# Optimization experiments

Hardware: AMD Instinct MI355X
Metric: run time of the kernel (lower is better)

The kernel has to match this reference:

```python
import jax, jax.numpy as jnp
import numpy as np

N = 50000
E = 800000
IN, HID, OUT = 256, 128, 64
BN_EPS = 1e-5

def sage(x, src, dst, Wl, bl, Wr):
    # PyG SAGEConv (aggr='mean'): lin_l(mean_j x_j) + lin_r(x_root)
    agg = jax.ops.segment_sum(x[src], dst, num_segments=N)
    deg = jax.ops.segment_sum(jnp.ones((src.shape[0], 1), x.dtype), dst, num_segments=N)
    mean_agg = agg / jnp.maximum(deg, 1.0)
    return mean_agg @ Wl + bl + x @ Wr

def bn_eval(x, gamma, beta):
    # eval-mode BatchNorm1d with running_mean=0, running_var=1
    return x * (gamma / jnp.sqrt(1.0 + BN_EPS)) + beta

def setup_inputs() -> dict:
    key = jax.random.key(0)
    ks = jax.random.split(key, 16)
    g = lambda k, shp, s: jax.random.normal(k, shp, jnp.float32) * s
    inp = {
        'x': g(ks[0], (N, IN), 1.0),
        'edge_index': jax.random.randint(ks[1], (2, E), 0, N, jnp.int32),
        'eps': g(ks[2], (10, N, OUT), 1.0),
        'W1l': g(ks[3], (IN, HID), 0.06), 'b1': jnp.zeros((HID,), jnp.float32), 'W1r': g(ks[4], (IN, HID), 0.06),
        'g1': jnp.ones((HID,), jnp.float32), 'be1': jnp.zeros((HID,), jnp.float32),
        'W2l': g(ks[5], (HID, 2 * HID), 0.09), 'b2': jnp.zeros((2 * HID,), jnp.float32), 'W2r': g(ks[6], (HID, 2 * HID), 0.09),
        'g2': jnp.ones((2 * HID,), jnp.float32), 'be2': jnp.zeros((2 * HID,), jnp.float32),
        'W3l': g(ks[7], (2 * HID, 2 * OUT), 0.06), 'b3': jnp.zeros((2 * OUT,), jnp.float32), 'W3r': g(ks[8], (2 * HID, 2 * OUT), 0.06),
        'Wd1': g(ks[9], (OUT, HID), 0.12), 'bd1': jnp.zeros((HID,), jnp.float32),
        'g3': jnp.ones((HID,), jnp.float32), 'be3': jnp.zeros((HID,), jnp.float32),
        'Wd2': g(ks[10], (HID, IN), 0.09), 'bd2': jnp.zeros((IN,), jnp.float32),
    }
    return inp

def reference(x, edge_index, eps, W1l, b1, W1r, g1, be1, W2l, b2, W2r, g2, be2,
              W3l, b3, W3r, Wd1, bd1, g3, be3, Wd2, bd2):
    src, dst = edge_index[0], edge_index[1]
    # encode (dropout is identity in eval mode)
    x1 = bn_eval(jax.nn.relu(sage(x, src, dst, W1l, b1, W1r)), g1, be1)
    x2 = bn_eval(jax.nn.relu(sage(x1, src, dst, W2l, b2, W2r)), g2, be2)
    mz = sage(x2, src, dst, W3l, b3, W3r)
    mean, log_std = mz[:, :OUT], mz[:, OUT:]
    # reparameterize: average of n_samples draws == mean + std * mean(eps)
    std = jnp.exp(log_std)
    z = mean + std * jnp.mean(eps, axis=0)
    # decode
    h = bn_eval(jax.nn.relu(z @ Wd1 + bd1), g3, be3) + x1
    return h @ Wd2 + bd2
```

## Files before the change

kernel.cpp:

```cpp
#include <hip/hip_runtime.h>


typedef unsigned short u16;
typedef short bf16x8 __attribute__((ext_vector_type(8)));
typedef float f32x4  __attribute__((ext_vector_type(4)));

constexpr float BN_EPS = 1e-5f;

__device__ __forceinline__ u16 f2bf(float f) {
    unsigned u = __float_as_uint(f);
    return (u16)((u + 0x7FFFu + ((u >> 16) & 1u)) >> 16);
}
__device__ __forceinline__ float bf2f(u16 h) {
    return __uint_as_float(((unsigned)h) << 16);
}
__device__ __forceinline__ void gl_lds16(const void* g, void* l) {
    __builtin_amdgcn_global_load_lds(
        (const __attribute__((address_space(1))) unsigned*)g,
        (__attribute__((address_space(3))) unsigned*)l, 16, 0, 0);
}

template<int KS>
__device__ __forceinline__ void stage_panel(const u16* g, char* lb, int k0, int t) {
    const int sr   = t >> 2;
    const int sq   = (t & 3) ^ ((t >> 3) & 3);
    const int wave = t >> 6;
    gl_lds16(g + (size_t)sr * KS + k0 + sq * 8,        lb + wave * 1024);
    gl_lds16(g + (size_t)(sr + 64) * KS + k0 + sq * 8, lb + 4096 + wave * 1024);
}


__global__ void histpack(const int* __restrict__ dst, int E, int* __restrict__ deg,
                         const float* __restrict__ x,
                         const float* __restrict__ W1l, const float* __restrict__ W1r,
                         const float* __restrict__ W2l, const float* __restrict__ W2r,
                         const float* __restrict__ W3l, const float* __restrict__ W3r,
                         const float* __restrict__ Wd1, const float* __restrict__ Wd2,
                         u16* __restrict__ Bt1, u16* __restrict__ Bt2,
                         u16* __restrict__ Bt3, u16* __restrict__ Btd1,
                         u16* __restrict__ Btd2, u16* __restrict__ xb,
                         int N, int Mpad) {
    int idx = blockIdx.x * 256 + threadIdx.x;
    if (idx < E) atomicAdd(&deg[dst[idx]], 1);
    if (idx < 65536) {
        int c = idx >> 8, k = idx & 255;
        float v = (c < 128) ? W1l[k * 128 + c] : W1r[k * 128 + (c - 128)];
        Bt1[c * 256 + k] = f2bf(v);
    } else if (idx < 131072) {
        int i2 = idx - 65536;
        int c = i2 >> 8, k = i2 & 255;
        float v = (k < 128) ? W2l[k * 256 + c] : W2r[(k - 128) * 256 + c];
        Bt2[c * 256 + k] = f2bf(v);
    } else if (idx < 196608) {
        int i2 = idx - 131072;
        int c = i2 >> 8, k = i2 & 255;
        float v = (c < 128) ? W3l[k * 128 + c] : W3r[k * 128 + (c - 128)];
        Bt3[c * 256 + k] = f2bf(v);
    } else if (idx < 204800) {
        int i2 = idx - 196608;
        int c = i2 >> 6, k = i2 & 63;
        Btd1[i2] = f2bf(Wd1[k * 128 + c]);
    } else if (idx < 237568) {
        int i2 = idx - 204800;
        int c = i2 >> 7, k = i2 & 127;
        Btd2[i2] = f2bf(Wd2[k * 256 + c]);
    }
    if (idx < Mpad * 64) {
        int row = idx >> 6, q = idx & 63;
        float4 v = make_float4(0.f, 0.f, 0.f, 0.f);
        if (row < N) v = *(const float4*)&x[(size_t)row * 256 + q * 4];
        ushort4 o;
        o.x = f2bf(v.x); o.y = f2bf(v.y); o.z = f2bf(v.z); o.w = f2bf(v.w);
        *(ushort4*)&xb[(size_t)row * 256 + q * 4] = o;
    }
}

__global__ __launch_bounds__(256)
void scan_partial(const int* __restrict__ deg, int N, int* __restrict__ bsum) {
    __shared__ int sd[256];
    int i = blockIdx.x * 256 + threadIdx.x;
    int v = (i < N) ? deg[i] : 0;
    sd[threadIdx.x] = v;
    __syncthreads();
    for (int off = 128; off > 0; off >>= 1) {
        if (threadIdx.x < off) sd[threadIdx.x] += sd[threadIdx.x + off];
        __syncthreads();
    }
    if (threadIdx.x == 0) bsum[blockIdx.x] = sd[0];
}

__global__ __launch_bounds__(256)
void scan_final2(const int* __restrict__ deg, const int* __restrict__ bsum,
                 int N, int E, int* __restrict__ row_ptr, int* __restrict__ cursor,
                 float* __restrict__ inv_deg) {
    __shared__ int sd[256];
    int t = threadIdx.x;
    int partial = 0;
    for (int j = t; j < blockIdx.x; j += 256) partial += bsum[j];
    sd[t] = partial;
    __syncthreads();
    for (int off = 128; off > 0; off >>= 1) {
        if (t < off) sd[t] += sd[t + off];
        __syncthreads();
    }
    int base = sd[0];
    __syncthreads();
    int i = blockIdx.x * 256 + t;
    int d = (i < N) ? deg[i] : 0;
    sd[t] = d;
    __syncthreads();
    for (int off = 1; off < 256; off <<= 1) {
        int u = (t >= off) ? sd[t - off] : 0;
        __syncthreads();
        sd[t] += u;
        __syncthreads();
    }
    if (i < N) {
        int excl = base + sd[t] - d;
        row_ptr[i] = excl;
        cursor[i]  = excl;
        inv_deg[i] = 1.0f / (float)max(d, 1);
        if (i == N - 1) row_ptr[N] = E;
    }
}

__global__ void fill_kernel(const int* __restrict__ src, const int* __restrict__ dst,
                            int E, int* __restrict__ cursor, int* __restrict__ csr) {
    int e = blockIdx.x * 256 + threadIdx.x;
    if (e < E) {
        int p = atomicAdd(&cursor[dst[e]], 1);
        csr[p] = src[e];
    }
}


template<int K, int NC>
__global__ __launch_bounds__(256)
void mgemm(const u16* __restrict__ A, const u16* __restrict__ Bt,
           void* __restrict__ Cout, int M) {
    __shared__ char lds[32768];
    char* As0 = lds;
    char* As1 = lds + 8192;
    char* Bs0 = lds + 16384;
    char* Bs1 = lds + 24576;

    const int t = threadIdx.x;
    const int l = t & 63;
    const int wave = t >> 6;
    const int wr = wave >> 1, wc = wave & 1;
    const int lr = l & 15, kg = l >> 4;
    const int row0 = blockIdx.x * 128;
    const int col0 = blockIdx.y * 128;

    f32x4 acc[4][4];
    #pragma unroll
    for (int m = 0; m < 4; m++)
        #pragma unroll
        for (int n = 0; n < 4; n++)
            #pragma unroll
            for (int r = 0; r < 4; r++) acc[m][n][r] = 0.f;

    const u16* Ab = A  + (size_t)row0 * K;
    const u16* Bb = Bt + (size_t)col0 * K;

    stage_panel<K>(Ab, As0, 0, t);
    stage_panel<K>(Bb, Bs0, 0, t);
    __syncthreads();

    const int swz = (kg ^ ((lr >> 1) & 3)) << 4;
    constexpr int NT = K / 32;
    for (int ks = 0; ks < NT; ks++) {
        char* Ac = (ks & 1) ? As1 : As0;
        char* Bc = (ks & 1) ? Bs1 : Bs0;
        if (ks + 1 < NT) {
            stage_panel<K>(Ab, (ks & 1) ? As0 : As1, (ks + 1) * 32, t);
            stage_panel<K>(Bb, (ks & 1) ? Bs0 : Bs1, (ks + 1) * 32, t);
        }
        bf16x8 af[4], bfr[4];
        #pragma unroll
        for (int m = 0; m < 4; m++)
            af[m] = *(const bf16x8*)(Ac + wr * 4096 + m * 1024 + lr * 64 + swz);
        #pragma unroll
        for (int n = 0; n < 4; n++)
            bfr[n] = *(const bf16x8*)(Bc + wc * 4096 + n * 1024 + lr * 64 + swz);
        #pragma unroll
        for (int m = 0; m < 4; m++)
            #pragma unroll
            for (int n = 0; n < 4; n++)
                acc[m][n] = __builtin_amdgcn_mfma_f32_16x16x32_bf16(
                    af[m], bfr[n], acc[m][n], 0, 0, 0);
        __syncthreads();
    }

    const int colb = col0 + wc * 64;
    const int rowb = row0 + wr * 64;
    __syncthreads();

    char* rp = lds + wave * 4096;
    #pragma unroll
    for (int m = 0; m < 4; m++) {
        #pragma unroll
        for (int n = 0; n < 4; n++)
            #pragma unroll
            for (int r = 0; r < 4; r++) {
                int rl = kg * 4 + r, cl = n * 16 + lr;
                ((u16*)rp)[rl * 64 + cl] = f2bf(acc[m][n][r]);
            }
        u16* rph = (u16*)rp;
        #pragma unroll
        for (int hh = 0; hh < 2; hh++) {
            int rloc = hh * 8 + (l >> 3);
            int grow = rowb + m * 16 + rloc;
            bf16x8 v8 = *(bf16x8*)&rph[rloc * 64 + (l & 7) * 8];
            if (grow < M)
                *(bf16x8*)((u16*)Cout + (size_t)grow * NC + colb + (l & 7) * 8) = v8;
        }
    }
}


__global__ __launch_bounds__(256)
void gemm23(const u16* __restrict__ catX, const u16* __restrict__ Bt2,
            const u16* __restrict__ Bt3,
            const float* __restrict__ b2, const float* __restrict__ g2,
            const float* __restrict__ be2,
            u16* __restrict__ Y3, int M) {
    __shared__ char lds[73728];
    char* Ad0 = lds;
    char* Ad1 = lds + 4096;
    char* Bd0 = lds + 8192;
    char* Bd1 = lds + 8192 + 16384;
    char* hb  = lds + 40960;

    const int t = threadIdx.x;
    const int l = t & 63;
    const int wave = t >> 6;
    const int lr = l & 15, kg = l >> 4;
    const int row0 = blockIdx.x * 64;
    const int swz = (kg ^ ((lr >> 1) & 3)) << 4;
    const int sr = t >> 2;
    const int sq = (t & 3) ^ ((t >> 3) & 3);
    const float rs = rsqrtf(1.0f + BN_EPS);

    const u16* Ab = catX + (size_t)row0 * 256;

    auto stageA = [&](char* buf, int k0) {
        gl_lds16(Ab + (size_t)sr * 256 + k0 + sq * 8, buf + wave * 1024);
    };
    auto stageB = [&](const u16* Bt, char* buf, int k0) {
        #pragma unroll
        for (int q = 0; q < 4; q++)
            gl_lds16(Bt + (size_t)(q * 64 + sr) * 256 + k0 + sq * 8,
                     buf + q * 4096 + wave * 1024);
    };

    f32x4 acc[4][4];
    #pragma unroll
    for (int m = 0; m < 4; m++)
        #pragma unroll
        for (int n = 0; n < 4; n++)
            #pragma unroll
            for (int r = 0; r < 4; r++) acc[m][n][r] = 0.f;

    stageA(Ad0, 0);
    stageB(Bt2, Bd0, 0);
    __syncthreads();
    for (int ks = 0; ks < 8; ks++) {
        char* Ac = (ks & 1) ? Ad1 : Ad0;
        char* Bc = (ks & 1) ? Bd1 : Bd0;
        if (ks < 7) {
            stageA((ks & 1) ? Ad0 : Ad1, (ks + 1) * 32);
            stageB(Bt2, (ks & 1) ? Bd0 : Bd1, (ks + 1) * 32);
        }
        bf16x8 af[4], bfr[4];
        #pragma unroll
        for (int m = 0; m < 4; m++)
            af[m] = *(const bf16x8*)(Ac + m * 1024 + lr * 64 + swz);
        #pragma unroll
        for (int n = 0; n < 4; n++)
            bfr[n] = *(const bf16x8*)(Bc + wave * 4096 + n * 1024 + lr * 64 + swz);
        #pragma unroll
        for (int m = 0; m < 4; m++)
            #pragma unroll
            for (int n = 0; n < 4; n++)
                acc[m][n] = __builtin_amdgcn_mfma_f32_16x16x32_bf16(
                    af[m], bfr[n], acc[m][n], 0, 0, 0);
        __syncthreads();
    }

    stageB(Bt3, Bd0, 0);

    {
        float bia[4], gpr[4], bet[4];
        #pragma unroll
        for (int n = 0; n < 4; n++) {
            int c = wave * 64 + n * 16 + lr;
            bia[n] = b2[c];
            gpr[n] = g2[c] * rs;
            bet[n] = be2[c];
        }
        #pragma unroll
        for (int m = 0; m < 4; m++)
            #pragma unroll
            for (int n = 0; n < 4; n++)
                #pragma unroll
                for (int r = 0; r < 4; r++) {
                    int rl = m * 16 + kg * 4 + r;
                    int cl = wave * 64 + n * 16 + lr;
                    float v = acc[m][n][r] + bia[n];
                    v = fmaxf(v, 0.f) * gpr[n] + bet[n];
                    int slot = (cl >> 3) ^ (rl & 7);
                    ((u16*)(hb + rl * 512 + slot * 16))[cl & 7] = f2bf(v);
                }
    }
    __syncthreads();

    #pragma unroll
    for (int m = 0; m < 4; m++)
        #pragma unroll
        for (int n = 0; n < 4; n++)
            #pragma unroll
            for (int r = 0; r < 4; r++) acc[m][n][r] = 0.f;

    for (int ks = 0; ks < 8; ks++) {
        char* Bc = (ks & 1) ? Bd1 : Bd0;
        if (ks < 7) stageB(Bt3, (ks & 1) ? Bd0 : Bd1, (ks + 1) * 32);
        bf16x8 af[4], bfr[4];
        #pragma unroll
        for (int m = 0; m < 4; m++) {
            int row = m * 16 + lr;
            int s = (ks * 4 + kg) ^ (row & 7);
            af[m] = *(const bf16x8*)(hb + row * 512 + s * 16);
        }
        #pragma unroll
        for (int n = 0; n < 4; n++)
            bfr[n] = *(const bf16x8*)(Bc + wave * 4096 + n * 1024 + lr * 64 + swz);
        #pragma unroll
        for (int m = 0; m < 4; m++)
            #pragma unroll
            for (int n = 0; n < 4; n++)
                acc[m][n] = __builtin_amdgcn_mfma_f32_16x16x32_bf16(
                    af[m], bfr[n], acc[m][n], 0, 0, 0);
        __syncthreads();
    }

    char* rp = lds + wave * 4096;
    #pragma unroll
    for (int m = 0; m < 4; m++) {
        #pragma unroll
        for (int n = 0; n < 4; n++)
            #pragma unroll
            for (int r = 0; r < 4; r++) {
                int rl = kg * 4 + r, cl = n * 16 + lr;
                ((u16*)rp)[rl * 64 + cl] = f2bf(acc[m][n][r]);
            }
        u16* rph = (u16*)rp;
        #pragma unroll
        for (int hh = 0; hh < 2; hh++) {
            int rloc = hh * 8 + (l >> 3);
            int grow = row0 + m * 16 + rloc;
            bf16x8 v8 = *(bf16x8*)&rph[rloc * 64 + (l & 7) * 8];
            if (grow < M)
                *(bf16x8*)&Y3[(size_t)grow * 256 + wave * 64 + (l & 7) * 8] = v8;
        }
    }
}


__global__ __launch_bounds__(256)
void dec_fused(const u16* __restrict__ zb, const u16* __restrict__ Btd1,
               const u16* __restrict__ Btd2, const float* __restrict__ bd1,
               const float* __restrict__ g3, const float* __restrict__ be3,
               const u16* __restrict__ x1, const float* __restrict__ bd2,
               float* __restrict__ out, int M) {
    __shared__ char lds[65536];
    const int t = threadIdx.x;
    const int l = t & 63;
    const int wave = t >> 6;
    const int wr = wave >> 1, wc = wave & 1;
    const int lr = l & 15, kg = l >> 4;
    const int row0 = blockIdx.x * 128;
    const float rs = rsqrtf(1.0f + BN_EPS);
    const int swz = (kg ^ ((lr >> 1) & 3)) << 4;
    char* hb = lds + 32768;

    stage_panel<64>(zb + (size_t)row0 * 64, lds,         0, t);
    stage_panel<64>(zb + (size_t)row0 * 64, lds + 8192, 32, t);
    stage_panel<64>(Btd1, lds + 16384,  0, t);
    stage_panel<64>(Btd1, lds + 24576, 32, t);
    __syncthreads();

    f32x4 acc[4][4];
    #pragma unroll
    for (int m = 0; m < 4; m++)
        #pragma unroll
        for (int n = 0; n < 4; n++)
            #pragma unroll
            for (int r = 0; r < 4; r++) acc[m][n][r] = 0.f;

    #pragma unroll
    for (int ks = 0; ks < 2; ks++) {
        char* Ac = lds + ks * 8192;
        char* Bc = lds + 16384 + ks * 8192;
        bf16x8 af[4], bfr[4];
        #pragma unroll
        for (int m = 0; m < 4; m++)
            af[m] = *(const bf16x8*)(Ac + wr * 4096 + m * 1024 + lr * 64 + swz);
        #pragma unroll
        for (int n = 0; n < 4; n++)
            bfr[n] = *(const bf16x8*)(Bc + wc * 4096 + n * 1024 + lr * 64 + swz);
        #pragma unroll
        for (int m = 0; m < 4; m++)
            #pragma unroll
            for (int n = 0; n < 4; n++)
                acc[m][n] = __builtin_amdgcn_mfma_f32_16x16x32_bf16(
                    af[m], bfr[n], acc[m][n], 0, 0, 0);
    }

    {
        float bia[4], gpr[4], bet[4];
        #pragma unroll
        for (int n = 0; n < 4; n++) {
            int c = wc * 64 + n * 16 + lr;
            bia[n] = bd1[c];
            gpr[n] = g3[c] * rs;
            bet[n] = be3[c];
        }
        #pragma unroll
        for (int m = 0; m < 4; m++)
            #pragma unroll
            for (int n = 0; n < 4; n++)
                #pragma unroll
                for (int r = 0; r < 4; r++) {
                    int rl = wr * 64 + m * 16 + kg * 4 + r;
                    int cl = wc * 64 + n * 16 + lr;
                    float v = acc[m][n][r] + bia[n];
                    v = fmaxf(v, 0.f) * gpr[n] + bet[n];
                    v += bf2f(x1[(size_t)(row0 + rl) * 256 + cl]);
                    int slot = (cl >> 3) ^ (rl & 7);
                    ((u16*)(hb + rl * 256 + slot * 16))[cl & 7] = f2bf(v);
                }
    }
    __syncthreads();

    for (int ch = 0; ch < 2; ch++) {
        const u16* Bb2 = Btd2 + ch * 16384;
        stage_panel<128>(Bb2, lds, 0, t);
        #pragma unroll
        for (int m = 0; m < 4; m++)
            #pragma unroll
            for (int n = 0; n < 4; n++)
                #pragma unroll
                for (int r = 0; r < 4; r++) acc[m][n][r] = 0.f;
        __syncthreads();

        for (int ks = 0; ks < 4; ks++) {
            char* Bc = lds + (ks & 1) * 8192;
            if (ks + 1 < 4)
                stage_panel<128>(Bb2, lds + (((ks & 1) ^ 1) * 8192), (ks + 1) * 32, t);
            bf16x8 af[4], bfr[4];
            #pragma unroll
            for (int m = 0; m < 4; m++) {
                int row = wr * 64 + m * 16 + lr;
                int s = (ks * 4 + kg) ^ (row & 7);
                af[m] = *(const bf16x8*)(hb + row * 256 + s * 16);
            }
            #pragma unroll
            for (int n = 0; n < 4; n++)
                bfr[n] = *(const bf16x8*)(Bc + wc * 4096 + n * 1024 + lr * 64 + swz);
            #pragma unroll
            for (int m = 0; m < 4; m++)
                #pragma unroll
                for (int n = 0; n < 4; n++)
                    acc[m][n] = __builtin_amdgcn_mfma_f32_16x16x32_bf16(
                        af[m], bfr[n], acc[m][n], 0, 0, 0);
            __syncthreads();
        }

        const int colb = ch * 128 + wc * 64;
        const int rowb = row0 + wr * 64;
        float b2v[4];
        #pragma unroll
        for (int n = 0; n < 4; n++) b2v[n] = bd2[colb + n * 16 + lr];
        char* rp = lds + wave * 4096;
        #pragma unroll
        for (int m = 0; m < 4; m++) {
            #pragma unroll
            for (int n = 0; n < 4; n++)
                #pragma unroll
                for (int r = 0; r < 4; r++)
                    ((float*)rp)[(kg * 4 + r) * 64 + n * 16 + lr] = acc[m][n][r] + b2v[n];
            float* rpf = (float*)rp;
            #pragma unroll
            for (int rr = 0; rr < 4; rr++) {
                int rloc = rr * 4 + kg;
                int grow = rowb + m * 16 + rloc;
                if (grow < M) {
                    f32x4 v4 = *(f32x4*)&rpf[rloc * 64 + lr * 4];
                    *(f32x4*)&out[(size_t)grow * 256 + colb + lr * 4] = v4;
                }
            }
        }
        __syncthreads();
    }
}


__global__ __launch_bounds__(256)
void agg1_kernel(const u16* __restrict__ Y1, const int* __restrict__ row_ptr,
                 const int* __restrict__ csr, const float* __restrict__ inv_deg,
                 const float* __restrict__ b1, const float* __restrict__ g1,
                 const float* __restrict__ be1, u16* __restrict__ catX, int N) {
    int g   = (blockIdx.x * 256 + threadIdx.x) >> 4;
    int sub = threadIdx.x & 15;
    if (g >= N) return;
    int b = row_ptr[g], e = row_ptr[g + 1];
    const int off = sub * 8;
    float a[8] = {};
    int ee = b;
    for (; ee + 3 < e; ee += 4) {
        int j0 = csr[ee], j1 = csr[ee + 1], j2 = csr[ee + 2], j3 = csr[ee + 3];
        bf16x8 v0 = *(const bf16x8*)&Y1[(size_t)j0 * 256 + off];
        bf16x8 v1 = *(const bf16x8*)&Y1[(size_t)j1 * 256 + off];
        bf16x8 v2 = *(const bf16x8*)&Y1[(size_t)j2 * 256 + off];
        bf16x8 v3 = *(const bf16x8*)&Y1[(size_t)j3 * 256 + off];
        #pragma unroll
        for (int r = 0; r < 8; r++)
            a[r] += (bf2f((u16)v0[r]) + bf2f((u16)v1[r]))
                  + (bf2f((u16)v2[r]) + bf2f((u16)v3[r]));
    }
    for (; ee < e; ee++) {
        bf16x8 v0 = *(const bf16x8*)&Y1[(size_t)csr[ee] * 256 + off];
        #pragma unroll
        for (int r = 0; r < 8; r++) a[r] += bf2f((u16)v0[r]);
    }
    float id = inv_deg[g];
    bf16x8 u = *(const bf16x8*)&Y1[(size_t)g * 256 + 128 + off];
    const float rs = rsqrtf(1.0f + BN_EPS);
    bf16x8 o;
    #pragma unroll
    for (int r = 0; r < 8; r++) {
        int c = off + r;
        float v = a[r] * id + b1[c] + bf2f((u16)u[r]);
        v = fmaxf(v, 0.f);
        v = v * (g1[c] * rs) + be1[c];
        o[r] = (short)f2bf(v);
    }
    *(bf16x8*)&catX[(size_t)g * 256 + 128 + off] = o;
}

__global__ __launch_bounds__(256)
void agg2_kernel(const int* __restrict__ row_ptr, const int* __restrict__ csr,
                 const float* __restrict__ inv_deg, u16* __restrict__ catX, int N) {
    int g   = (blockIdx.x * 256 + threadIdx.x) >> 4;
    int sub = threadIdx.x & 15;
    if (g >= N) return;
    int b = row_ptr[g], e = row_ptr[g + 1];
    const int off = sub * 8;
    float a[8] = {};
    int ee = b;
    for (; ee + 3 < e; ee += 4) {
        int j0 = csr[ee], j1 = csr[ee + 1], j2 = csr[ee + 2], j3 = csr[ee + 3];
        bf16x8 v0 = *(const bf16x8*)&catX[(size_t)j0 * 256 + 128 + off];
        bf16x8 v1 = *(const bf16x8*)&catX[(size_t)j1 * 256 + 128 + off];
        bf16x8 v2 = *(const bf16x8*)&catX[(size_t)j2 * 256 + 128 + off];
        bf16x8 v3 = *(const bf16x8*)&catX[(size_t)j3 * 256 + 128 + off];
        #pragma unroll
        for (int r = 0; r < 8; r++)
            a[r] += (bf2f((u16)v0[r]) + bf2f((u16)v1[r]))
                  + (bf2f((u16)v2[r]) + bf2f((u16)v3[r]));
    }
    for (; ee < e; ee++) {
        bf16x8 v0 = *(const bf16x8*)&catX[(size_t)csr[ee] * 256 + 128 + off];
        #pragma unroll
        for (int r = 0; r < 8; r++) a[r] += bf2f((u16)v0[r]);
    }
    float id = inv_deg[g];
    bf16x8 o;
    #pragma unroll
    for (int r = 0; r < 8; r++) o[r] = (short)f2bf(a[r] * id);
    *(bf16x8*)&catX[(size_t)g * 256 + off] = o;
}

__global__ __launch_bounds__(256)
void agg3_kernel(const u16* __restrict__ Y3, const int* __restrict__ row_ptr,
                 const int* __restrict__ csr, const float* __restrict__ inv_deg,
                 const float* __restrict__ b3, const float* __restrict__ eps,
                 u16* __restrict__ z, int N) {
    int g   = (blockIdx.x * 256 + threadIdx.x) >> 4;
    int sub = threadIdx.x & 15;
    if (g >= N) return;
    int b = row_ptr[g], e = row_ptr[g + 1];
    const int off = sub * 8;

    f32x4 emv = {0.f, 0.f, 0.f, 0.f};
    #pragma unroll
    for (int t10 = 0; t10 < 10; t10++) {
        f32x4 v = *(const f32x4*)&eps[((size_t)t10 * N + g) * 64 + sub * 4];
        emv += v;
    }
    emv *= 0.1f;

    float a[8] = {};
    int ee = b;
    for (; ee + 3 < e; ee += 4) {
        int j0 = csr[ee], j1 = csr[ee + 1], j2 = csr[ee + 2], j3 = csr[ee + 3];
        bf16x8 v0 = *(const bf16x8*)&Y3[(size_t)j0 * 256 + off];
        bf16x8 v1 = *(const bf16x8*)&Y3[(size_t)j1 * 256 + off];
        bf16x8 v2 = *(const bf16x8*)&Y3[(size_t)j2 * 256 + off];
        bf16x8 v3 = *(const bf16x8*)&Y3[(size_t)j3 * 256 + off];
        #pragma unroll
        for (int r = 0; r < 8; r++)
            a[r] += (bf2f((u16)v0[r]) + bf2f((u16)v1[r]))
                  + (bf2f((u16)v2[r]) + bf2f((u16)v3[r]));
    }
    for (; ee < e; ee++) {
        bf16x8 v0 = *(const bf16x8*)&Y3[(size_t)csr[ee] * 256 + off];
        #pragma unroll
        for (int r = 0; r < 8; r++) a[r] += bf2f((u16)v0[r]);
    }
    float id = inv_deg[g];
    bf16x8 u = *(const bf16x8*)&Y3[(size_t)g * 256 + 128 + off];
    float mzv[8];
    #pragma unroll
    for (int r = 0; r < 8; r++)
        mzv[r] = a[r] * id + b3[off + r] + bf2f((u16)u[r]);

    const int wl = threadIdx.x & 63;
    const int wb = wl & ~15;
    const int s0 = wb + ((2 * sub) & 15);
    const int s1 = wb + ((2 * sub + 1) & 15);
    float em8[8];
    #pragma unroll
    for (int q = 0; q < 4; q++) {
        em8[q]     = __shfl(emv[q], s0);
        em8[4 + q] = __shfl(emv[q], s1);
    }
    float hi[8];
    #pragma unroll
    for (int r = 0; r < 8; r++) hi[r] = __shfl_xor(mzv[r], 8);

    if (sub < 8) {
        bf16x8 o;
        #pragma unroll
        for (int r = 0; r < 8; r++)
            o[r] = (short)f2bf(mzv[r] + expf(hi[r]) * em8[r]);
        *(bf16x8*)&z[(size_t)g * 64 + sub * 8] = o;
    }
}


extern "C" void kernel_launch(void* const* d_in, const int* in_sizes, int n_in,
                              void* d_out, int out_size, void* d_ws, size_t ws_size,
                              hipStream_t stream) {
    const float* x    = (const float*)d_in[0];
    const int*   ei   = (const int*)d_in[1];
    const float* eps  = (const float*)d_in[2];
    const float* W1l  = (const float*)d_in[3];
    const float* b1   = (const float*)d_in[4];
    const float* W1r  = (const float*)d_in[5];
    const float* g1   = (const float*)d_in[6];
    const float* be1  = (const float*)d_in[7];
    const float* W2l  = (const float*)d_in[8];
    const float* b2   = (const float*)d_in[9];
    const float* W2r  = (const float*)d_in[10];
    const float* g2   = (const float*)d_in[11];
    const float* be2  = (const float*)d_in[12];
    const float* W3l  = (const float*)d_in[13];
    const float* b3   = (const float*)d_in[14];
    const float* W3r  = (const float*)d_in[15];
    const float* Wd1  = (const float*)d_in[16];
    const float* bd1  = (const float*)d_in[17];
    const float* g3   = (const float*)d_in[18];
    const float* be3  = (const float*)d_in[19];
    const float* Wd2  = (const float*)d_in[20];
    const float* bd2  = (const float*)d_in[21];

    const int Nn   = in_sizes[0] / 256;
    const int E    = in_sizes[1] / 2;
    const int Mpad = ((Nn + 127) / 128) * 128;
    const int* srcp = ei;
    const int* dstp = ei + E;
    const int nb = (Nn + 255) / 256;

    char* w = (char*)d_ws;
    auto alloc = [&](size_t bytes) -> void* {
        void* p = (void*)w;
        w += (bytes + 255) & ~(size_t)255;
        return p;
    };
    int*   deg     = (int*)  alloc((size_t)Nn * 4);
    int*   bsum    = (int*)  alloc((size_t)nb * 4);
    int*   row_ptr = (int*)  alloc((size_t)(Nn + 1) * 4);
    int*   cursor  = (int*)  alloc((size_t)Nn * 4);
    float* inv_deg = (float*)alloc((size_t)Nn * 4);
    int*   csr     = (int*)  alloc((size_t)E * 4);
    u16*   Bt1     = (u16*)  alloc(256 * 256 * 2);
    u16*   Bt2     = (u16*)  alloc(256 * 256 * 2);
    u16*   Bt3     = (u16*)  alloc(256 * 256 * 2);
    u16*   Btd1    = (u16*)  alloc(128 * 64 * 2);
    u16*   Btd2    = (u16*)  alloc(256 * 128 * 2);
    u16*   xb      = (u16*)  alloc((size_t)Mpad * 256 * 2);
    u16*   zb      = (u16*)  alloc((size_t)Mpad * 64 * 2);
    u16*   bufA    = (u16*)  alloc((size_t)Mpad * 256 * 2);
    u16*   bufB    = (u16*)  alloc((size_t)Mpad * 256 * 2);
    u16*   bufC    = (u16*)  alloc((size_t)Mpad * 256 * 2);
    if ((size_t)(w - (char*)d_ws) > ws_size) return;

    hipMemsetAsync(deg, 0, (size_t)Nn * 4, stream);
    histpack<<<(Mpad * 64 + 255) / 256, 256, 0, stream>>>(
        dstp, E, deg, x, W1l, W1r, W2l, W2r, W3l, W3r, Wd1, Wd2,
        Bt1, Bt2, Bt3, Btd1, Btd2, xb, Nn, Mpad);
    scan_partial<<<nb, 256, 0, stream>>>(deg, Nn, bsum);
    scan_final2<<<nb, 256, 0, stream>>>(deg, bsum, Nn, E, row_ptr, cursor, inv_deg);
    fill_kernel<<<(E + 255) / 256, 256, 0, stream>>>(srcp, dstp, E, cursor, csr);

    dim3 g2c(Mpad / 128, 2);
    const int aggBlocks = (Nn + 15) / 16;

    mgemm<256, 256><<<g2c, 256, 0, stream>>>(xb, Bt1, bufA, Mpad);
    agg1_kernel<<<aggBlocks, 256, 0, stream>>>(bufA, row_ptr, csr, inv_deg,
                                               b1, g1, be1, bufB, Nn);
    agg2_kernel<<<aggBlocks, 256, 0, stream>>>(row_ptr, csr, inv_deg, bufB, Nn);
    gemm23<<<Mpad / 64, 256, 0, stream>>>(bufB, Bt2, Bt3, b2, g2, be2, bufC, Mpad);
    agg3_kernel<<<aggBlocks, 256, 0, stream>>>(bufC, row_ptr, csr, inv_deg,
                                               b3, eps, zb, Nn);
    dec_fused<<<Mpad / 128, 256, 0, stream>>>(
        zb, Btd1, Btd2, bd1, g3, be3, bufB + 128, bd2, (float*)d_out, Nn);
}
```

Before: 282.2 us.

## Fuse layer-2 aggregation into gemm23 and layer-3 aggregation into decoder

The layer-2 neighbor mean aggregation now runs inside the layer-2/3 GEMM kernel. The gathered rows are written straight into a padded LDS A-tile instead of round-tripping through global memory. Likewise, the layer-3 aggregation, reparameterization and eps averaging are folded into the decoder kernel, so the z buffer and two launches go away. The cost is that the irregular gather work now sits inside GEMM blocks, with a larger LDS footprint and less parallelism per gather, which may reduce occupancy and latency hiding.

```diff
diff --git a/kernel.cpp b/kernel.cpp
--- a/kernel.cpp
+++ b/kernel.cpp
@@ -220,293 +220,6 @@
 
 
 __global__ __launch_bounds__(256)
-void gemm23(const u16* __restrict__ catX, const u16* __restrict__ Bt2,
-            const u16* __restrict__ Bt3,
-            const float* __restrict__ b2, const float* __restrict__ g2,
-            const float* __restrict__ be2,
-            u16* __restrict__ Y3, int M) {
-    __shared__ char lds[73728];
-    char* Ad0 = lds;
-    char* Ad1 = lds + 4096;
-    char* Bd0 = lds + 8192;
-    char* Bd1 = lds + 8192 + 16384;
-    char* hb  = lds + 40960;
-
-    const int t = threadIdx.x;
-    const int l = t & 63;
-    const int wave = t >> 6;
-    const int lr = l & 15, kg = l >> 4;
-    const int row0 = blockIdx.x * 64;
-    const int swz = (kg ^ ((lr >> 1) & 3)) << 4;
-    const int sr = t >> 2;
-    const int sq = (t & 3) ^ ((t >> 3) & 3);
-    const float rs = rsqrtf(1.0f + BN_EPS);
-
-    const u16* Ab = catX + (size_t)row0 * 256;
-
-    auto stageA = [&](char* buf, int k0) {
-        gl_lds16(Ab + (size_t)sr * 256 + k0 + sq * 8, buf + wave * 1024);
-    };
-    auto stageB = [&](const u16* Bt, char* buf, int k0) {
-        #pragma unroll
-        for (int q = 0; q < 4; q++)
-            gl_lds16(Bt + (size_t)(q * 64 + sr) * 256 + k0 + sq * 8,
-                     buf + q * 4096 + wave * 1024);
-    };
-
-    f32x4 acc[4][4];
-    #pragma unroll
-    for (int m = 0; m < 4; m++)
-        #pragma unroll
-        for (int n = 0; n < 4; n++)
-            #pragma unroll
-            for (int r = 0; r < 4; r++) acc[m][n][r] = 0.f;
-
-    stageA(Ad0, 0);
-    stageB(Bt2, Bd0, 0);
-    __syncthreads();
-    for (int ks = 0; ks < 8; ks++) {
-        char* Ac = (ks & 1) ? Ad1 : Ad0;
-        char* Bc = (ks & 1) ? Bd1 : Bd0;
-        if (ks < 7) {
-            stageA((ks & 1) ? Ad0 : Ad1, (ks + 1) * 32);
-            stageB(Bt2, (ks & 1) ? Bd0 : Bd1, (ks + 1) * 32);
-        }
-        bf16x8 af[4], bfr[4];
-        #pragma unroll
-        for (int m = 0; m < 4; m++)
-            af[m] = *(const bf16x8*)(Ac + m * 1024 + lr * 64 + swz);
-        #pragma unroll
-        for (int n = 0; n < 4; n++)
-            bfr[n] = *(const bf16x8*)(Bc + wave * 4096 + n * 1024 + lr * 64 + swz);
-        #pragma unroll
-        for (int m = 0; m < 4; m++)
-            #pragma unroll
-            for (int n = 0; n < 4; n++)
-                acc[m][n] = __builtin_amdgcn_mfma_f32_16x16x32_bf16(
-                    af[m], bfr[n], acc[m][n], 0, 0, 0);
-        __syncthreads();
-    }
-
-    stageB(Bt3, Bd0, 0);
-
-    {
-        float bia[4], gpr[4], bet[4];
-        #pragma unroll
-        for (int n = 0; n < 4; n++) {
-            int c = wave * 64 + n * 16 + lr;
-            bia[n] = b2[c];
-            gpr[n] = g2[c] * rs;
-            bet[n] = be2[c];
-        }
-        #pragma unroll
-        for (int m = 0; m < 4; m++)
-            #pragma unroll
-            for (int n = 0; n < 4; n++)
-                #pragma unroll
-                for (int r = 0; r < 4; r++) {
-                    int rl = m * 16 + kg * 4 + r;
-                    int cl = wave * 64 + n * 16 + lr;
-                    float v = acc[m][n][r] + bia[n];
-                    v = fmaxf(v, 0.f) * gpr[n] + bet[n];
-                    int slot = (cl >> 3) ^ (rl & 7);
-                    ((u16*)(hb + rl * 512 + slot * 16))[cl & 7] = f2bf(v);
-                }
-    }
-    __syncthreads();
-
-    #pragma unroll
-    for (int m = 0; m < 4; m++)
-        #pragma unroll
-        for (int n = 0; n < 4; n++)
-            #pragma unroll
-            for (int r = 0; r < 4; r++) acc[m][n][r] = 0.f;
-
-    for (int ks = 0; ks < 8; ks++) {
-        char* Bc = (ks & 1) ? Bd1 : Bd0;
-        if (ks < 7) stageB(Bt3, (ks & 1) ? Bd0 : Bd1, (ks + 1) * 32);
-        bf16x8 af[4], bfr[4];
-        #pragma unroll
-        for (int m = 0; m < 4; m++) {
-            int row = m * 16 + lr;
-            int s = (ks * 4 + kg) ^ (row & 7);
-            af[m] = *(const bf16x8*)(hb + row * 512 + s * 16);
-        }
-        #pragma unroll
-        for (int n = 0; n < 4; n++)
-            bfr[n] = *(const bf16x8*)(Bc + wave * 4096 + n * 1024 + lr * 64 + swz);
-        #pragma unroll
-        for (int m = 0; m < 4; m++)
-            #pragma unroll
-            for (int n = 0; n < 4; n++)
-                acc[m][n] = __builtin_amdgcn_mfma_f32_16x16x32_bf16(
-                    af[m], bfr[n], acc[m][n], 0, 0, 0);
-        __syncthreads();
-    }
-
-    char* rp = lds + wave * 4096;
-    #pragma unroll
-    for (int m = 0; m < 4; m++) {
-        #pragma unroll
-        for (int n = 0; n < 4; n++)
-            #pragma unroll
-            for (int r = 0; r < 4; r++) {
-                int rl = kg * 4 + r, cl = n * 16 + lr;
-                ((u16*)rp)[rl * 64 + cl] = f2bf(acc[m][n][r]);
-            }
-        u16* rph = (u16*)rp;
-        #pragma unroll
-        for (int hh = 0; hh < 2; hh++) {
-            int rloc = hh * 8 + (l >> 3);
-            int grow = row0 + m * 16 + rloc;
-            bf16x8 v8 = *(bf16x8*)&rph[rloc * 64 + (l & 7) * 8];
-            if (grow < M)
-                *(bf16x8*)&Y3[(size_t)grow * 256 + wave * 64 + (l & 7) * 8] = v8;
-        }
-    }
-}
-
-
-__global__ __launch_bounds__(256)
-void dec_fused(const u16* __restrict__ zb, const u16* __restrict__ Btd1,
-               const u16* __restrict__ Btd2, const float* __restrict__ bd1,
-               const float* __restrict__ g3, const float* __restrict__ be3,
-               const u16* __restrict__ x1, const float* __restrict__ bd2,
-               float* __restrict__ out, int M) {
-    __shared__ char lds[65536];
-    const int t = threadIdx.x;
-    const int l = t & 63;
-    const int wave = t >> 6;
-    const int wr = wave >> 1, wc = wave & 1;
-    const int lr = l & 15, kg = l >> 4;
-    const int row0 = blockIdx.x * 128;
-    const float rs = rsqrtf(1.0f + BN_EPS);
-    const int swz = (kg ^ ((lr >> 1) & 3)) << 4;
-    char* hb = lds + 32768;
-
-    stage_panel<64>(zb + (size_t)row0 * 64, lds,         0, t);
-    stage_panel<64>(zb + (size_t)row0 * 64, lds + 8192, 32, t);
-    stage_panel<64>(Btd1, lds + 16384,  0, t);
-    stage_panel<64>(Btd1, lds + 24576, 32, t);
-    __syncthreads();
-
-    f32x4 acc[4][4];
-    #pragma unroll
-    for (int m = 0; m < 4; m++)
-        #pragma unroll
-        for (int n = 0; n < 4; n++)
-            #pragma unroll
-            for (int r = 0; r < 4; r++) acc[m][n][r] = 0.f;
-
-    #pragma unroll
-    for (int ks = 0; ks < 2; ks++) {
-        char* Ac = lds + ks * 8192;
-        char* Bc = lds + 16384 + ks * 8192;
-        bf16x8 af[4], bfr[4];
-        #pragma unroll
-        for (int m = 0; m < 4; m++)
-            af[m] = *(const bf16x8*)(Ac + wr * 4096 + m * 1024 + lr * 64 + swz);
-        #pragma unroll
-        for (int n = 0; n < 4; n++)
-            bfr[n] = *(const bf16x8*)(Bc + wc * 4096 + n * 1024 + lr * 64 + swz);
-        #pragma unroll
-        for (int m = 0; m < 4; m++)
-            #pragma unroll
-            for (int n = 0; n < 4; n++)
-                acc[m][n] = __builtin_amdgcn_mfma_f32_16x16x32_bf16(
-                    af[m], bfr[n], acc[m][n], 0, 0, 0);
-    }
-
-    {
-        float bia[4], gpr[4], bet[4];
-        #pragma unroll
-        for (int n = 0; n < 4; n++) {
-            int c = wc * 64 + n * 16 + lr;
-            bia[n] = bd1[c];
-            gpr[n] = g3[c] * rs;
-            bet[n] = be3[c];
-        }
-        #pragma unroll
-        for (int m = 0; m < 4; m++)
-            #pragma unroll
-            for (int n = 0; n < 4; n++)
-                #pragma unroll
-                for (int r = 0; r < 4; r++) {
-                    int rl = wr * 64 + m * 16 + kg * 4 + r;
-                    int cl = wc * 64 + n * 16 + lr;
-                    float v = acc[m][n][r] + bia[n];
-                    v = fmaxf(v, 0.f) * gpr[n] + bet[n];
-                    v += bf2f(x1[(size_t)(row0 + rl) * 256 + cl]);
-                    int slot = (cl >> 3) ^ (rl & 7);
-                    ((u16*)(hb + rl * 256 + slot * 16))[cl & 7] = f2bf(v);
-                }
-    }
-    __syncthreads();
-
-    for (int ch = 0; ch < 2; ch++) {
-        const u16* Bb2 = Btd2 + ch * 16384;
-        stage_panel<128>(Bb2, lds, 0, t);
-        #pragma unroll
-        for (int m = 0; m < 4; m++)
-            #pragma unroll
-            for (int n = 0; n < 4; n++)
-                #pragma unroll
-                for (int r = 0; r < 4; r++) acc[m][n][r] = 0.f;
-        __syncthreads();
-
-        for (int ks = 0; ks < 4; ks++) {
-            char* Bc = lds + (ks & 1) * 8192;
-            if (ks + 1 < 4)
-                stage_panel<128>(Bb2, lds + (((ks & 1) ^ 1) * 8192), (ks + 1) * 32, t);
-            bf16x8 af[4], bfr[4];
-            #pragma unroll
-            for (int m = 0; m < 4; m++) {
-                int row = wr * 64 + m * 16 + lr;
-                int s = (ks * 4 + kg) ^ (row & 7);
-                af[m] = *(const bf16x8*)(hb + row * 256 + s * 16);
-            }
-            #pragma unroll
-            for (int n = 0; n < 4; n++)
-                bfr[n] = *(const bf16x8*)(Bc + wc * 4096 + n * 1024 + lr * 64 + swz);
-            #pragma unroll
-            for (int m = 0; m < 4; m++)
-                #pragma unroll
-                for (int n = 0; n < 4; n++)
-                    acc[m][n] = __builtin_amdgcn_mfma_f32_16x16x32_bf16(
-                        af[m], bfr[n], acc[m][n], 0, 0, 0);
-            __syncthreads();
-        }
-
-        const int colb = ch * 128 + wc * 64;
-        const int rowb = row0 + wr * 64;
-        float b2v[4];
-        #pragma unroll
-        for (int n = 0; n < 4; n++) b2v[n] = bd2[colb + n * 16 + lr];
-        char* rp = lds + wave * 4096;
-        #pragma unroll
-        for (int m = 0; m < 4; m++) {
-            #pragma unroll
-            for (int n = 0; n < 4; n++)
-                #pragma unroll
-                for (int r = 0; r < 4; r++)
-                    ((float*)rp)[(kg * 4 + r) * 64 + n * 16 + lr] = acc[m][n][r] + b2v[n];
-            float* rpf = (float*)rp;
-            #pragma unroll
-            for (int rr = 0; rr < 4; rr++) {
-                int rloc = rr * 4 + kg;
-                int grow = rowb + m * 16 + rloc;
-                if (grow < M) {
-                    f32x4 v4 = *(f32x4*)&rpf[rloc * 64 + lr * 4];
-                    *(f32x4*)&out[(size_t)grow * 256 + colb + lr * 4] = v4;
-                }
-            }
-        }
-        __syncthreads();
-    }
-}
-
-
-__global__ __launch_bounds__(256)
 void agg1_kernel(const u16* __restrict__ Y1, const int* __restrict__ row_ptr,
                  const int* __restrict__ csr, const float* __restrict__ inv_deg,
                  const float* __restrict__ b1, const float* __restrict__ g1,
@@ -549,103 +262,392 @@
     *(bf16x8*)&catX[(size_t)g * 256 + 128 + off] = o;
 }
 
+
 __global__ __launch_bounds__(256)
-void agg2_kernel(const int* __restrict__ row_ptr, const int* __restrict__ csr,
-                 const float* __restrict__ inv_deg, u16* __restrict__ catX, int N) {
-    int g   = (blockIdx.x * 256 + threadIdx.x) >> 4;
-    int sub = threadIdx.x & 15;
-    if (g >= N) return;
-    int b = row_ptr[g], e = row_ptr[g + 1];
+void gemm23f(const u16* __restrict__ catX, const u16* __restrict__ Bt2,
+             const u16* __restrict__ Bt3,
+             const int* __restrict__ row_ptr, const int* __restrict__ csr,
+             const float* __restrict__ inv_deg,
+             const float* __restrict__ b2, const float* __restrict__ g2,
+             const float* __restrict__ be2,
+             u16* __restrict__ Y3, int Nn, int M) {
+    __shared__ char lds[66560];
+    char* At  = lds;
+    char* Bd0 = lds + 33792;
+    char* Bd1 = lds + 50176;
+
+    const int t = threadIdx.x;
+    const int l = t & 63;
+    const int wave = t >> 6;
+    const int lr = l & 15, kg = l >> 4;
+    const int row0 = blockIdx.x * 64;
+    const int swz = (kg ^ ((lr >> 1) & 3)) << 4;
+    const int sr = t >> 2;
+    const int sq = (t & 3) ^ ((t >> 3) & 3);
+    const float rs = rsqrtf(1.0f + BN_EPS);
+
+    auto stageB = [&](const u16* Bt, char* buf, int k0) {
+        #pragma unroll
+        for (int q = 0; q < 4; q++)
+            gl_lds16(Bt + (size_t)(q * 64 + sr) * 256 + k0 + sq * 8,
+                     buf + q * 4096 + wave * 1024);
+    };
+
+    stageB(Bt2, Bd0, 0);
+
+    const int grp = t >> 4, sub = t & 15;
     const int off = sub * 8;
-    float a[8] = {};
-    int ee = b;
-    for (; ee + 3 < e; ee += 4) {
-        int j0 = csr[ee], j1 = csr[ee + 1], j2 = csr[ee + 2], j3 = csr[ee + 3];
-        bf16x8 v0 = *(const bf16x8*)&catX[(size_t)j0 * 256 + 128 + off];
-        bf16x8 v1 = *(const bf16x8*)&catX[(size_t)j1 * 256 + 128 + off];
-        bf16x8 v2 = *(const bf16x8*)&catX[(size_t)j2 * 256 + 128 + off];
-        bf16x8 v3 = *(const bf16x8*)&catX[(size_t)j3 * 256 + 128 + off];
-        #pragma unroll
-        for (int r = 0; r < 8; r++)
-            a[r] += (bf2f((u16)v0[r]) + bf2f((u16)v1[r]))
-                  + (bf2f((u16)v2[r]) + bf2f((u16)v3[r]));
-    }
-    for (; ee < e; ee++) {
-        bf16x8 v0 = *(const bf16x8*)&catX[(size_t)csr[ee] * 256 + 128 + off];
-        #pragma unroll
-        for (int r = 0; r < 8; r++) a[r] += bf2f((u16)v0[r]);
-    }
-    float id = inv_deg[g];
-    bf16x8 o;
+    for (int q = 0; q < 4; q++) {
+        int gl = grp * 4 + q;
+        int g  = row0 + gl;
+        float a[8] = {};
+        if (g < Nn) {
+            int b = row_ptr[g], e = row_ptr[g + 1];
+            int ee = b;
+            for (; ee + 3 < e; ee += 4) {
+                int j0 = csr[ee], j1 = csr[ee + 1], j2 = csr[ee + 2], j3 = csr[ee + 3];
+                bf16x8 v0 = *(const bf16x8*)&catX[(size_t)j0 * 256 + 128 + off];
+                bf16x8 v1 = *(const bf16x8*)&catX[(size_t)j1 * 256 + 128 + off];
+                bf16x8 v2 = *(const bf16x8*)&catX[(size_t)j2 * 256 + 128 + off];
+                bf16x8 v3 = *(const bf16x8*)&catX[(size_t)j3 * 256 + 128 + off];
+                #pragma unroll
+                for (int r = 0; r < 8; r++)
+                    a[r] += (bf2f((u16)v0[r]) + bf2f((u16)v1[r]))
+                          + (bf2f((u16)v2[r]) + bf2f((u16)v3[r]));
+            }
+            for (; ee < e; ee++) {
+                bf16x8 v0 = *(const bf16x8*)&catX[(size_t)csr[ee] * 256 + 128 + off];
+                #pragma unroll
+                for (int r = 0; r < 8; r++) a[r] += bf2f((u16)v0[r]);
+            }
+            float id = inv_deg[g];
+            #pragma unroll
+            for (int r = 0; r < 8; r++) a[r] *= id;
+        }
+        bf16x8 o;
+        #pragma unroll
+        for (int r = 0; r < 8; r++) o[r] = (short)f2bf(a[r]);
+        *(bf16x8*)(At + gl * 528 + sub * 16) = o;
+    }
+    {
+        int row = t >> 2;
+        size_t g = (size_t)(row0 + row);
+        #pragma unroll
+        for (int s = 0; s < 4; s++) {
+            int slot = (t & 3) + s * 4;
+            bf16x8 v = *(const bf16x8*)&catX[g * 256 + 128 + slot * 8];
+            *(bf16x8*)(At + row * 528 + 256 + slot * 16) = v;
+        }
+    }
+    __syncthreads();
+
+    f32x4 acc[4][4];
     #pragma unroll
-    for (int r = 0; r < 8; r++) o[r] = (short)f2bf(a[r] * id);
-    *(bf16x8*)&catX[(size_t)g * 256 + off] = o;
-}
+    for (int m = 0; m < 4; m++)
+        #pragma unroll
+        for (int n = 0; n < 4; n++)
+            #pragma unroll
+            for (int r = 0; r < 4; r++) acc[m][n][r] = 0.f;
+
+    for (int ks = 0; ks < 8; ks++) {
+        char* Bc = (ks & 1) ? Bd1 : Bd0;
+        if (ks < 7) stageB(Bt2, (ks & 1) ? Bd0 : Bd1, (ks + 1) * 32);
+        bf16x8 af[4], bfr[4];
+        #pragma unroll
+        for (int m = 0; m < 4; m++)
+            af[m] = *(const bf16x8*)(At + (m * 16 + lr) * 528 + ks * 64 + kg * 16);
+        #pragma unroll
+        for (int n = 0; n < 4; n++)
+            bfr[n] = *(const bf16x8*)(Bc + wave * 4096 + n * 1024 + lr * 64 + swz);
+        #pragma unroll
+        for (int m = 0; m < 4; m++)
+            #pragma unroll
+            for (int n = 0; n < 4; n++)
+                acc[m][n] = __builtin_amdgcn_mfma_f32_16x16x32_bf16(
+                    af[m], bfr[n], acc[m][n], 0, 0, 0);
+        __syncthreads();
+    }
+
+    stageB(Bt3, Bd0, 0);
+
+    {
+        float bia[4], gpr[4], bet[4];
+        #pragma unroll
+        for (int n = 0; n < 4; n++) {
+            int c = wave * 64 + n * 16 + lr;
+            bia[n] = b2[c];
+            gpr[n] = g2[c] * rs;
+            bet[n] = be2[c];
+        }
+        #pragma unroll
+        for (int m = 0; m < 4; m++)
+            #pragma unroll
+            for (int n = 0; n < 4; n++)
+                #pragma unroll
+                for (int r = 0; r < 4; r++) {
+                    int rl = m * 16 + kg * 4 + r;
+                    int cl = wave * 64 + n * 16 + lr;
+                    float v = acc[m][n][r] + bia[n];
+                    v = fmaxf(v, 0.f) * gpr[n] + bet[n];
+                    *(u16*)(At + rl * 528 + cl * 2) = f2bf(v);
+                }
+    }
+    __syncthreads();
+
+    #pragma unroll
+    for (int m = 0; m < 4; m++)
+        #pragma unroll
+        for (int n = 0; n < 4; n++)
+            #pragma unroll
+            for (int r = 0; r < 4; r++) acc[m][n][r] = 0.f;
+
+    for (int ks = 0; ks < 8; ks++) {
+        char* Bc = (ks & 1) ? Bd1 : Bd0;
+        if (ks < 7) stageB(Bt3, (ks & 1) ? Bd0 : Bd1, (ks + 1) * 32);
+        bf16x8 af[4], bfr[4];
+        #pragma unroll
+        for (int m = 0; m < 4; m++)
+            af[m] = *(const bf16x8*)(At + (m * 16 + lr) * 528 + ks * 64 + kg * 16);
+        #pragma unroll
+        for (int n = 0; n < 4; n++)
+            bfr[n] = *(const bf16x8*)(Bc + wave * 4096 + n * 1024 + lr * 64 + swz);
+        #pragma unroll
+        for (int m = 0; m < 4; m++)
+            #pragma unroll
+            for (int n = 0; n < 4; n++)
+                acc[m][n] = __builtin_amdgcn_mfma_f32_16x16x32_bf16(
+                    af[m], bfr[n], acc[m][n], 0, 0, 0);
+        __syncthreads();
+    }
+
+    char* rp = lds + wave * 4096;
+    #pragma unroll
+    for (int m = 0; m < 4; m++) {
+        #pragma unroll
+        for (int n = 0; n < 4; n++)
+            #pragma unroll
+            for (int r = 0; r < 4; r++) {
+                int rl = kg * 4 + r, cl = n * 16 + lr;
+                ((u16*)rp)[rl * 64 + cl] = f2bf(acc[m][n][r]);
+            }
+        u16* rph = (u16*)rp;
+        #pragma unroll
+        for (int hh = 0; hh < 2; hh++) {
+            int rloc = hh * 8 + (l >> 3);
+            int grow = row0 + m * 16 + rloc;
+            bf16x8 v8 = *(bf16x8*)&rph[rloc * 64 + (l & 7) * 8];
+            if (grow < M)
+                *(bf16x8*)&Y3[(size_t)grow * 256 + wave * 64 + (l & 7) * 8] = v8;
+        }
+    }
+}
+
 
 __global__ __launch_bounds__(256)
-void agg3_kernel(const u16* __restrict__ Y3, const int* __restrict__ row_ptr,
-                 const int* __restrict__ csr, const float* __restrict__ inv_deg,
-                 const float* __restrict__ b3, const float* __restrict__ eps,
-                 u16* __restrict__ z, int N) {
-    int g   = (blockIdx.x * 256 + threadIdx.x) >> 4;
-    int sub = threadIdx.x & 15;
-    if (g >= N) return;
-    int b = row_ptr[g], e = row_ptr[g + 1];
+void decf(const u16* __restrict__ Y3, const int* __restrict__ row_ptr,
+          const int* __restrict__ csr, const float* __restrict__ inv_deg,
+          const float* __restrict__ b3, const float* __restrict__ eps,
+          const u16* __restrict__ Btd1, const u16* __restrict__ Btd2,
+          const float* __restrict__ bd1, const float* __restrict__ g3,
+          const float* __restrict__ be3, const u16* __restrict__ x1,
+          const float* __restrict__ bd2, float* __restrict__ out,
+          int Nn, int M) {
+    __shared__ char lds[67584];
+    char* zl = lds + 16384;
+    char* hb = lds + 34816;
+    const int t = threadIdx.x;
+    const int l = t & 63;
+    const int wave = t >> 6;
+    const int wr = wave >> 1, wc = wave & 1;
+    const int lr = l & 15, kg = l >> 4;
+    const int row0 = blockIdx.x * 128;
+    const float rs = rsqrtf(1.0f + BN_EPS);
+    const int swz = (kg ^ ((lr >> 1) & 3)) << 4;
+
+    stage_panel<64>(Btd1, lds,        0, t);
+    stage_panel<64>(Btd1, lds + 8192, 32, t);
+
+    const int grp = t >> 4, sub = t & 15;
     const int off = sub * 8;
-
-    f32x4 emv = {0.f, 0.f, 0.f, 0.f};
-    #pragma unroll
-    for (int t10 = 0; t10 < 10; t10++) {
-        f32x4 v = *(const f32x4*)&eps[((size_t)t10 * N + g) * 64 + sub * 4];
-        emv += v;
-    }
-    emv *= 0.1f;
-
-    float a[8] = {};
-    int ee = b;
-    for (; ee + 3 < e; ee += 4) {
-        int j0 = csr[ee], j1 = csr[ee + 1], j2 = csr[ee + 2], j3 = csr[ee + 3];
-        bf16x8 v0 = *(const bf16x8*)&Y3[(size_t)j0 * 256 + off];
-        bf16x8 v1 = *(const bf16x8*)&Y3[(size_t)j1 * 256 + off];
-        bf16x8 v2 = *(const bf16x8*)&Y3[(size_t)j2 * 256 + off];
-        bf16x8 v3 = *(const bf16x8*)&Y3[(size_t)j3 * 256 + off];
-        #pragma unroll
-        for (int r = 0; r < 8; r++)
-            a[r] += (bf2f((u16)v0[r]) + bf2f((u16)v1[r]))
-                  + (bf2f((u16)v2[r]) + bf2f((u16)v3[r]));
-    }
-    for (; ee < e; ee++) {
-        bf16x8 v0 = *(const bf16x8*)&Y3[(size_t)csr[ee] * 256 + off];
-        #pragma unroll
-        for (int r = 0; r < 8; r++) a[r] += bf2f((u16)v0[r]);
-    }
-    float id = inv_deg[g];
-    bf16x8 u = *(const bf16x8*)&Y3[(size_t)g * 256 + 128 + off];
-    float mzv[8];
-    #pragma unroll
-    for (int r = 0; r < 8; r++)
-        mzv[r] = a[r] * id + b3[off + r] + bf2f((u16)u[r]);
-
-    const int wl = threadIdx.x & 63;
-    const int wb = wl & ~15;
+    const int wb = (t & 63) & ~15;
     const int s0 = wb + ((2 * sub) & 15);
     const int s1 = wb + ((2 * sub + 1) & 15);
-    float em8[8];
+    for (int q = 0; q < 8; q++) {
+        int gl = grp * 8 + q;
+        int g  = row0 + gl;
+        if (g < Nn) {
+            f32x4 emv = {0.f, 0.f, 0.f, 0.f};
+            #pragma unroll
+            for (int t10 = 0; t10 < 10; t10++) {
+                f32x4 v = *(const f32x4*)&eps[((size_t)t10 * Nn + g) * 64 + sub * 4];
+                emv += v;
+            }
+            emv *= 0.1f;
+
+            float a[8] = {};
+            int b = row_ptr[g], e = row_ptr[g + 1];
+            int ee = b;
+            for (; ee + 3 < e; ee += 4) {
+                int j0 = csr[ee], j1 = csr[ee + 1], j2 = csr[ee + 2], j3 = csr[ee + 3];
+                bf16x8 v0 = *(const bf16x8*)&Y3[(size_t)j0 * 256 + off];
+                bf16x8 v1 = *(const bf16x8*)&Y3[(size_t)j1 * 256 + off];
+                bf16x8 v2 = *(const bf16x8*)&Y3[(size_t)j2 * 256 + off];
+                bf16x8 v3 = *(const bf16x8*)&Y3[(size_t)j3 * 256 + off];
+                #pragma unroll
+                for (int r = 0; r < 8; r++)
+                    a[r] += (bf2f((u16)v0[r]) + bf2f((u16)v1[r]))
+                          + (bf2f((u16)v2[r]) + bf2f((u16)v3[r]));
+            }
+            for (; ee < e; ee++) {
+                bf16x8 v0 = *(const bf16x8*)&Y3[(size_t)csr[ee] * 256 + off];
+                #pragma unroll
+                for (int r = 0; r < 8; r++) a[r] += bf2f((u16)v0[r]);
+            }
+            float id = inv_deg[g];
+            bf16x8 u = *(const bf16x8*)&Y3[(size_t)g * 256 + 128 + off];
+            float mzv[8];
+            #pragma unroll
+            for (int r = 0; r < 8; r++)
+                mzv[r] = a[r] * id + b3[off + r] + bf2f((u16)u[r]);
+
+            float em8[8];
+            #pragma unroll
+            for (int qq = 0; qq < 4; qq++) {
+                em8[qq]     = __shfl(emv[qq], s0);
+                em8[4 + qq] = __shfl(emv[qq], s1);
+            }
+            float hi[8];
+            #pragma unroll
+            for (int r = 0; r < 8; r++) hi[r] = __shfl_xor(mzv[r], 8);
+
+            if (sub < 8) {
+                bf16x8 o;
+                #pragma unroll
+                for (int r = 0; r < 8; r++)
+                    o[r] = (short)f2bf(mzv[r] + expf(hi[r]) * em8[r]);
+                *(bf16x8*)(zl + gl * 144 + sub * 16) = o;
+            }
+        } else if (sub < 8) {
+            bf16x8 o;
+            #pragma unroll
+            for (int r = 0; r < 8; r++) o[r] = 0;
+            *(bf16x8*)(zl + gl * 144 + sub * 16) = o;
+        }
+    }
+    __syncthreads();
+
+    f32x4 acc[4][4];
     #pragma unroll
-    for (int q = 0; q < 4; q++) {
-        em8[q]     = __shfl(emv[q], s0);
-        em8[4 + q] = __shfl(emv[q], s1);
-    }
-    float hi[8];
+    for (int m = 0; m < 4; m++)
+        #pragma unroll
+        for (int n = 0; n < 4; n++)
+            #pragma unroll
+            for (int r = 0; r < 4; r++) acc[m][n][r] = 0.f;
+
     #pragma unroll
-    for (int r = 0; r < 8; r++) hi[r] = __shfl_xor(mzv[r], 8);
-
-    if (sub < 8) {
-        bf16x8 o;
-        #pragma unroll
-        for (int r = 0; r < 8; r++)
-            o[r] = (short)f2bf(mzv[r] + expf(hi[r]) * em8[r]);
-        *(bf16x8*)&z[(size_t)g * 64 + sub * 8] = o;
+    for (int ks = 0; ks < 2; ks++) {
+        char* Bc = lds + ks * 8192;
+        bf16x8 af[4], bfr[4];
+        #pragma unroll
+        for (int m = 0; m < 4; m++)
+            af[m] = *(const bf16x8*)(zl + (wr * 64 + m * 16 + lr) * 144
+                                        + ks * 64 + kg * 16);
+        #pragma unroll
+        for (int n = 0; n < 4; n++)
+            bfr[n] = *(const bf16x8*)(Bc + wc * 4096 + n * 1024 + lr * 64 + swz);
+        #pragma unroll
+        for (int m = 0; m < 4; m++)
+            #pragma unroll
+            for (int n = 0; n < 4; n++)
+                acc[m][n] = __builtin_amdgcn_mfma_f32_16x16x32_bf16(
+                    af[m], bfr[n], acc[m][n], 0, 0, 0);
+    }
+
+    {
+        float bia[4], gpr[4], bet[4];
+        #pragma unroll
+        for (int n = 0; n < 4; n++) {
+            int c = wc * 64 + n * 16 + lr;
+            bia[n] = bd1[c];
+            gpr[n] = g3[c] * rs;
+            bet[n] = be3[c];
+        }
+        #pragma unroll
+        for (int m = 0; m < 4; m++)
+            #pragma unroll
+            for (int n = 0; n < 4; n++)
+                #pragma unroll
+                for (int r = 0; r < 4; r++) {
+                    int rl = wr * 64 + m * 16 + kg * 4 + r;
+                    int cl = wc * 64 + n * 16 + lr;
+                    float v = acc[m][n][r] + bia[n];
+                    v = fmaxf(v, 0.f) * gpr[n] + bet[n];
+                    v += bf2f(x1[(size_t)(row0 + rl) * 256 + cl]);
+                    int slot = (cl >> 3) ^ (rl & 7);
+                    ((u16*)(hb + rl * 256 + slot * 16))[cl & 7] = f2bf(v);
+                }
+    }
+    __syncthreads();
+
+    for (int ch = 0; ch < 2; ch++) {
+        const u16* Bb2 = Btd2 + ch * 16384;
+        stage_panel<128>(Bb2, lds, 0, t);
+        #pragma unroll
+        for (int m = 0; m < 4; m++)
+            #pragma unroll
+            for (int n = 0; n < 4; n++)
+                #pragma unroll
+                for (int r = 0; r < 4; r++) acc[m][n][r] = 0.f;
+        __syncthreads();
+
+        for (int ks = 0; ks < 4; ks++) {
+            char* Bc = lds + (ks & 1) * 8192;
+            if (ks + 1 < 4)
+                stage_panel<128>(Bb2, lds + (((ks & 1) ^ 1) * 8192), (ks + 1) * 32, t);
+            bf16x8 af[4], bfr[4];
+            #pragma unroll
+            for (int m = 0; m < 4; m++) {
+                int row = wr * 64 + m * 16 + lr;
+                int s = (ks * 4 + kg) ^ (row & 7);
+                af[m] = *(const bf16x8*)(hb + row * 256 + s * 16);
+            }
+            #pragma unroll
+            for (int n = 0; n < 4; n++)
+                bfr[n] = *(const bf16x8*)(Bc + wc * 4096 + n * 1024 + lr * 64 + swz);
+            #pragma unroll
+            for (int m = 0; m < 4; m++)
+                #pragma unroll
+                for (int n = 0; n < 4; n++)
+                    acc[m][n] = __builtin_amdgcn_mfma_f32_16x16x32_bf16(
+                        af[m], bfr[n], acc[m][n], 0, 0, 0);
+            __syncthreads();
+        }
+
+        const int colb = ch * 128 + wc * 64;
+        const int rowb = row0 + wr * 64;
+        float b2v[4];
+        #pragma unroll
+        for (int n = 0; n < 4; n++) b2v[n] = bd2[colb + n * 16 + lr];
+        char* rp = lds + wave * 4096;
+        #pragma unroll
+        for (int m = 0; m < 4; m++) {
+            #pragma unroll
+            for (int n = 0; n < 4; n++)
+                #pragma unroll
+                for (int r = 0; r < 4; r++)
+                    ((float*)rp)[(kg * 4 + r) * 64 + n * 16 + lr] = acc[m][n][r] + b2v[n];
+            float* rpf = (float*)rp;
+            #pragma unroll
+            for (int rr = 0; rr < 4; rr++) {
+                int rloc = rr * 4 + kg;
+                int grow = rowb + m * 16 + rloc;
+                if (grow < M) {
+                    f32x4 v4 = *(f32x4*)&rpf[rloc * 64 + lr * 4];
+                    *(f32x4*)&out[(size_t)grow * 256 + colb + lr * 4] = v4;
+                }
+            }
+        }
+        __syncthreads();
     }
 }
 
@@ -701,7 +703,6 @@
     u16*   Btd1    = (u16*)  alloc(128 * 64 * 2);
     u16*   Btd2    = (u16*)  alloc(256 * 128 * 2);
     u16*   xb      = (u16*)  alloc((size_t)Mpad * 256 * 2);
-    u16*   zb      = (u16*)  alloc((size_t)Mpad * 64 * 2);
     u16*   bufA    = (u16*)  alloc((size_t)Mpad * 256 * 2);
     u16*   bufB    = (u16*)  alloc((size_t)Mpad * 256 * 2);
     u16*   bufC    = (u16*)  alloc((size_t)Mpad * 256 * 2);
@@ -721,10 +722,9 @@
     mgemm<256, 256><<<g2c, 256, 0, stream>>>(xb, Bt1, bufA, Mpad);
     agg1_kernel<<<aggBlocks, 256, 0, stream>>>(bufA, row_ptr, csr, inv_deg,
                                                b1, g1, be1, bufB, Nn);
-    agg2_kernel<<<aggBlocks, 256, 0, stream>>>(row_ptr, csr, inv_deg, bufB, Nn);
-    gemm23<<<Mpad / 64, 256, 0, stream>>>(bufB, Bt2, Bt3, b2, g2, be2, bufC, Mpad);
-    agg3_kernel<<<aggBlocks, 256, 0, stream>>>(bufC, row_ptr, csr, inv_deg,
-                                               b3, eps, zb, Nn);
-    dec_fused<<<Mpad / 128, 256, 0, stream>>>(
-        zb, Btd1, Btd2, bd1, g3, be3, bufB + 128, bd2, (float*)d_out, Nn);
-}
+    gemm23f<<<Mpad / 64, 256, 0, stream>>>(bufB, Bt2, Bt3, row_ptr, csr, inv_deg,
+                                           b2, g2, be2, bufC, Nn, Mpad);
+    decf<<<Mpad / 128, 256, 0, stream>>>(bufC, row_ptr, csr, inv_deg, b3, eps,
+                                         Btd1, Btd2, bd1, g3, be3,
+                                         bufB + 128, bd2, (float*)d_out, Nn, Nn);
+}
```

New measurement: 328.5 us. 1.16x slower.
